# Kernel tuning notes

Measured on AMD Instinct MI355X. Metric: run time of the kernel, lower is better.

Reference implementation:

```python
import jax, jax.numpy as jnp
import numpy as np

N_WIRES = 4
DIM = 2 ** N_WIRES          # 16-dim state vector
N_OPS = 30                  # RandomLayer(n_ops=30)
GAMMA = 1.0
ALPHA = 0.5
C64 = jnp.complex64


def _rx_mat(t):
    h = t / 2
    c = jnp.cos(h).astype(C64)
    s = (-1j * jnp.sin(h)).astype(C64)
    return jnp.stack([jnp.stack([c, s]), jnp.stack([s, c])])


def _ry_mat(t):
    h = t / 2
    c = jnp.cos(h).astype(C64)
    s = jnp.sin(h).astype(C64)
    return jnp.stack([jnp.stack([c, -s]), jnp.stack([s, c])])


def _rz_mat(t):
    h = (t / 2).astype(C64)
    z = jnp.zeros((), C64)
    return jnp.stack([jnp.stack([jnp.exp(-1j * h), z]), jnp.stack([z, jnp.exp(1j * h)])])


def _embed(g, w):
    # kron(I_{2^w}, g, I_{2^{n-1-w}}); wire 0 = most significant qubit
    return jnp.kron(jnp.kron(jnp.eye(2 ** w, dtype=C64), g),
                    jnp.eye(2 ** (N_WIRES - 1 - w), dtype=C64))


def _cnot_full(c, t):
    m = np.zeros((DIM, DIM), np.complex64)
    for i in range(DIM):
        j = i ^ (1 << (N_WIRES - 1 - t)) if (i >> (N_WIRES - 1 - c)) & 1 else i
        m[j, i] = 1.0
    return jnp.asarray(m)


def fixed_unitary(rand_angles, rx_param, ry_param):
    """Compose the whole batch-independent gate sequence (random layer +
    per-wire trainable RX/RY) into one 16x16 unitary — the 'fused kernel'."""
    U = jnp.eye(DIM, dtype=C64)
    for i in range(N_OPS):
        t, w = i % 4, i % N_WIRES
        if t == 0:
            g = _embed(_rx_mat(rand_angles[i]), w)
        elif t == 1:
            g = _embed(_ry_mat(rand_angles[i]), w)
        elif t == 2:
            g = _embed(_rz_mat(rand_angles[i]), w)
        else:
            g = _cnot_full(w, (w + 1) % N_WIRES)
        U = g @ U
    for w in range(N_WIRES):
        U = _embed(_rx_mat(rx_param[0]), w) @ U
        U = _embed(_ry_mat(ry_param[0]), w) @ U
    return U


def encode_ry(state, angles):
    """GeneralEncoder '4xRy': apply RY(angles[:, w]) on wire w, batched."""
    B = state.shape[0]
    for w in range(N_WIRES):
        h = angles[:, w] / 2
        c = jnp.cos(h).astype(C64)[:, None, None]
        s = jnp.sin(h).astype(C64)[:, None, None]
        st = state.reshape(B, 2 ** w, 2, 2 ** (N_WIRES - 1 - w))
        s0, s1 = st[:, :, 0, :], st[:, :, 1, :]
        state = jnp.stack([c * s0 - s * s1, s * s0 + c * s1], axis=2).reshape(B, DIM)
    return state


def setup_inputs() -> dict:
    key = jax.random.key(0)
    k1, k2, k3, k4, k5 = jax.random.split(key, 5)
    B = 1048576
    return {
        "x": jax.random.normal(k1, (B, 4), dtype=jnp.float32),
        "y": jax.random.normal(k2, (B, 4), dtype=jnp.float32),
        "rand_angles": jax.random.uniform(k3, (30,), dtype=jnp.float32),
        "rx_param": jax.random.normal(k4, (1,), dtype=jnp.float32),
        "ry_param": jax.random.normal(k5, (1,), dtype=jnp.float32),
    }


def reference(x, y, rand_angles, rx_param, ry_param):
    B = x.shape[0]
    # classical RBF kernel, [B, 1]
    diff = x - y
    rbf = jnp.exp(-GAMMA * jnp.sum(diff * diff, axis=-1, keepdims=True))
    # quantum kernel: |0..0> -> encode(x) -> fixed unitary -> encode(-y)
    state = jnp.zeros((B, DIM), C64).at[:, 0].set(1.0)
    state = encode_ry(state, x)
    U = fixed_unitary(rand_angles, rx_param, ry_param)
    state = jnp.einsum('ij,bj->bi', U, state)
    state = encode_ry(state, -y)
    # torch: abs(states.view(-1)[0]) — first amplitude of first batch element
    qk = jnp.abs(state.reshape(-1)[0])
    return ALPHA * rbf + (1.0 - ALPHA) * qk
```

## Files before the change

### kernel.cpp

```cpp
#include <hip/hip_runtime.h>
#include <math.h>

#define DIM 16
#define N_OPS 30

__global__ __launch_bounds__(64) void build_qk_kernel(
    const float* __restrict__ x, const float* __restrict__ y,
    const float* __restrict__ rand_angles, const float* __restrict__ rx_param,
    const float* __restrict__ ry_param, float* __restrict__ qk_out) {
    const int lane = threadIdx.x;

    float h = 0.0f;
    if (lane < N_OPS)           h = 0.5f * rand_angles[lane];
    else if (lane == 30)        h = 0.5f * rx_param[0];
    else if (lane == 31)        h = 0.5f * ry_param[0];
    else if (lane >= 32 && lane < 36) h = 0.5f * x[lane - 32];
    else if (lane >= 36 && lane < 40) h = 0.5f * y[lane - 36];
    float sh_l, ch_l;
    __sincosf(h, &sh_l, &ch_l);

    float sr = 1.0f, si = 0.0f;
    #pragma unroll
    for (int w = 0; w < 4; ++w) {
        const int p = 3 - w;
        const float cw = __shfl(ch_l, 32 + w);
        const float sw = __shfl(sh_l, 32 + w);
        sr *= ((lane >> p) & 1) ? sw : cw;
    }

    #pragma unroll
    for (int i = 0; i < N_OPS; ++i) {
        const int t = i & 3;
        const float ch = __shfl(ch_l, i);
        const float sh = __shfl(sh_l, i);
        if (t == 0) {
            const float pr = __shfl_xor(sr, 8);
            const float pi = __shfl_xor(si, 8);
            const float nr = ch * sr + sh * pi;
            const float ni = ch * si - sh * pr;
            sr = nr; si = ni;
        } else if (t == 1) {
            const float pr = __shfl_xor(sr, 4);
            const float pi = __shfl_xor(si, 4);
            const float sg = ((lane >> 2) & 1) ? sh : -sh;
            const float nr = ch * sr + sg * pr;
            const float ni = ch * si + sg * pi;
            sr = nr; si = ni;
        } else if (t == 2) {
            const float sg = ((lane >> 1) & 1) ? sh : -sh;
            const float nr = ch * sr - sg * si;
            const float ni = ch * si + sg * sr;
            sr = nr; si = ni;
        } else {
            const float pr = __shfl_xor(sr, 8);
            const float pi = __shfl_xor(si, 8);
            if (lane & 1) { sr = pr; si = pi; }
        }
    }

    const float chx = __shfl(ch_l, 30), shx = __shfl(sh_l, 30);
    const float chy = __shfl(ch_l, 31), shy = __shfl(sh_l, 31);
    #pragma unroll
    for (int w = 0; w < 4; ++w) {
        const int p = 3 - w;
        {
            const float pr = __shfl_xor(sr, 1 << p);
            const float pi = __shfl_xor(si, 1 << p);
            const float nr = chx * sr + shx * pi;
            const float ni = chx * si - shx * pr;
            sr = nr; si = ni;
        }
        {
            const float pr = __shfl_xor(sr, 1 << p);
            const float pi = __shfl_xor(si, 1 << p);
            const float sg = ((lane >> p) & 1) ? shy : -shy;
            const float nr = chy * sr + sg * pr;
            const float ni = chy * si + sg * pi;
            sr = nr; si = ni;
        }
    }

    float wy = 1.0f;
    #pragma unroll
    for (int w = 0; w < 4; ++w) {
        const int p = 3 - w;
        const float cw = __shfl(ch_l, 36 + w);
        const float sw = __shfl(sh_l, 36 + w);
        wy *= ((lane >> p) & 1) ? sw : cw;
    }
    float ar = wy * sr;
    float ai = wy * si;
    #pragma unroll
    for (int m = 8; m >= 1; m >>= 1) {
        ar += __shfl_xor(ar, m);
        ai += __shfl_xor(ai, m);
    }
    if (lane == 0) qk_out[0] = sqrtf(ar * ar + ai * ai);
}

__global__ __launch_bounds__(256) void rbf_out_kernel(
    const float4* __restrict__ x, const float4* __restrict__ y,
    const float* __restrict__ qk_ptr, float* __restrict__ out, int B) {
    const int idx = blockIdx.x * blockDim.x + threadIdx.x;
    if (idx >= B) return;
    const float half_qk = 0.5f * qk_ptr[0];
    const float4 xv = x[idx];
    const float4 yv = y[idx];
    const float dx = xv.x - yv.x;
    const float dy = xv.y - yv.y;
    const float dz = xv.z - yv.z;
    const float dw = xv.w - yv.w;
    const float ss = dx * dx + dy * dy + dz * dz + dw * dw;
    out[idx] = 0.5f * expf(-ss) + half_qk;
}

extern "C" void kernel_launch(void* const* d_in, const int* in_sizes, int n_in,
                              void* d_out, int out_size, void* d_ws, size_t ws_size,
                              hipStream_t stream) {
    const float* x = (const float*)d_in[0];
    const float* y = (const float*)d_in[1];
    const float* rand_angles = (const float*)d_in[2];
    const float* rx_param = (const float*)d_in[3];
    const float* ry_param = (const float*)d_in[4];
    float* out = (float*)d_out;
    float* qk = (float*)d_ws;

    const int B = in_sizes[0] / 4;

    build_qk_kernel<<<1, 64, 0, stream>>>(x, y, rand_angles, rx_param, ry_param, qk);

    const int blocks = (B + 255) / 256;
    rbf_out_kernel<<<blocks, 256, 0, stream>>>(
        (const float4*)x, (const float4*)y, qk, out, B);
}
```

Baseline: 83.24 us.

## Fuse quantum-kernel scalar computation into RBF kernel, recomputed per block

Merges the single-wave quantum amplitude kernel and the elementwise RBF kernel into one launch. Every block's first wave recomputes the 16-amplitude state simulation redundantly and shares the result through shared memory, while the RBF values for two elements per thread are computed in parallel. This removes one kernel launch and the serial dependency between the two launches. The cost is redundant shuffle-heavy work and a block barrier in each of 2048 blocks. The change also switches expf to the fast __expf intrinsic, which lowers precision.

```diff
diff --git a/kernel.cpp b/kernel.cpp
--- a/kernel.cpp
+++ b/kernel.cpp
@@ -4,114 +4,127 @@
 #define DIM 16
 #define N_OPS 30
 
-__global__ __launch_bounds__(64) void build_qk_kernel(
+__global__ __launch_bounds__(256) void fused_hybrid_kernel(
+    const float4* __restrict__ x4, const float4* __restrict__ y4,
     const float* __restrict__ x, const float* __restrict__ y,
     const float* __restrict__ rand_angles, const float* __restrict__ rx_param,
-    const float* __restrict__ ry_param, float* __restrict__ qk_out) {
-    const int lane = threadIdx.x;
+    const float* __restrict__ ry_param, float* __restrict__ out, int B) {
+    __shared__ float s_qk;
 
-    float h = 0.0f;
-    if (lane < N_OPS)           h = 0.5f * rand_angles[lane];
-    else if (lane == 30)        h = 0.5f * rx_param[0];
-    else if (lane == 31)        h = 0.5f * ry_param[0];
-    else if (lane >= 32 && lane < 36) h = 0.5f * x[lane - 32];
-    else if (lane >= 36 && lane < 40) h = 0.5f * y[lane - 36];
-    float sh_l, ch_l;
-    __sincosf(h, &sh_l, &ch_l);
+    const int tid = threadIdx.x;
+    const int i0 = blockIdx.x * 512 + tid;
+    const int i1 = i0 + 256;
 
-    float sr = 1.0f, si = 0.0f;
-    #pragma unroll
-    for (int w = 0; w < 4; ++w) {
-        const int p = 3 - w;
-        const float cw = __shfl(ch_l, 32 + w);
-        const float sw = __shfl(sh_l, 32 + w);
-        sr *= ((lane >> p) & 1) ? sw : cw;
+    float r0 = 0.0f, r1 = 0.0f;
+    if (i0 < B) {
+        const float4 xv = x4[i0];
+        const float4 yv = y4[i0];
+        const float dx = xv.x - yv.x, dy = xv.y - yv.y;
+        const float dz = xv.z - yv.z, dw = xv.w - yv.w;
+        r0 = 0.5f * __expf(-(dx * dx + dy * dy + dz * dz + dw * dw));
+    }
+    if (i1 < B) {
+        const float4 xv = x4[i1];
+        const float4 yv = y4[i1];
+        const float dx = xv.x - yv.x, dy = xv.y - yv.y;
+        const float dz = xv.z - yv.z, dw = xv.w - yv.w;
+        r1 = 0.5f * __expf(-(dx * dx + dy * dy + dz * dz + dw * dw));
     }
 
-    #pragma unroll
-    for (int i = 0; i < N_OPS; ++i) {
-        const int t = i & 3;
-        const float ch = __shfl(ch_l, i);
-        const float sh = __shfl(sh_l, i);
-        if (t == 0) {
-            const float pr = __shfl_xor(sr, 8);
-            const float pi = __shfl_xor(si, 8);
-            const float nr = ch * sr + sh * pi;
-            const float ni = ch * si - sh * pr;
-            sr = nr; si = ni;
-        } else if (t == 1) {
-            const float pr = __shfl_xor(sr, 4);
-            const float pi = __shfl_xor(si, 4);
-            const float sg = ((lane >> 2) & 1) ? sh : -sh;
-            const float nr = ch * sr + sg * pr;
-            const float ni = ch * si + sg * pi;
-            sr = nr; si = ni;
-        } else if (t == 2) {
-            const float sg = ((lane >> 1) & 1) ? sh : -sh;
-            const float nr = ch * sr - sg * si;
-            const float ni = ch * si + sg * sr;
-            sr = nr; si = ni;
-        } else {
-            const float pr = __shfl_xor(sr, 8);
-            const float pi = __shfl_xor(si, 8);
-            if (lane & 1) { sr = pr; si = pi; }
+    if (tid < 64) {
+        const int lane = tid;
+        float h = 0.0f;
+        if (lane < N_OPS)                 h = 0.5f * rand_angles[lane];
+        else if (lane == 30)              h = 0.5f * rx_param[0];
+        else if (lane == 31)              h = 0.5f * ry_param[0];
+        else if (lane >= 32 && lane < 36) h = 0.5f * x[lane - 32];
+        else if (lane >= 36 && lane < 40) h = 0.5f * y[lane - 36];
+        float sh_l, ch_l;
+        __sincosf(h, &sh_l, &ch_l);
+
+        float sr = 1.0f, si = 0.0f;
+        #pragma unroll
+        for (int w = 0; w < 4; ++w) {
+            const int p = 3 - w;
+            const float cw = __shfl(ch_l, 32 + w);
+            const float sw = __shfl(sh_l, 32 + w);
+            sr *= ((lane >> p) & 1) ? sw : cw;
         }
+
+        #pragma unroll
+        for (int i = 0; i < N_OPS; ++i) {
+            const int t = i & 3;
+            const float ch = __shfl(ch_l, i);
+            const float sh = __shfl(sh_l, i);
+            if (t == 0) {
+                const float pr = __shfl_xor(sr, 8);
+                const float pi = __shfl_xor(si, 8);
+                const float nr = ch * sr + sh * pi;
+                const float ni = ch * si - sh * pr;
+                sr = nr; si = ni;
+            } else if (t == 1) {
+                const float pr = __shfl_xor(sr, 4);
+                const float pi = __shfl_xor(si, 4);
+                const float sg = ((lane >> 2) & 1) ? sh : -sh;
+                const float nr = ch * sr + sg * pr;
+                const float ni = ch * si + sg * pi;
+                sr = nr; si = ni;
+            } else if (t == 2) {
+                const float sg = ((lane >> 1) & 1) ? sh : -sh;
+                const float nr = ch * sr - sg * si;
+                const float ni = ch * si + sg * sr;
+                sr = nr; si = ni;
+            } else {
+                const float pr = __shfl_xor(sr, 8);
+                const float pi = __shfl_xor(si, 8);
+                if (lane & 1) { sr = pr; si = pi; }
+            }
+        }
+
+        const float chx = __shfl(ch_l, 30), shx = __shfl(sh_l, 30);
+        const float chy = __shfl(ch_l, 31), shy = __shfl(sh_l, 31);
+        #pragma unroll
+        for (int w = 0; w < 4; ++w) {
+            const int p = 3 - w;
+            {
+                const float pr = __shfl_xor(sr, 1 << p);
+                const float pi = __shfl_xor(si, 1 << p);
+                const float nr = chx * sr + shx * pi;
+                const float ni = chx * si - shx * pr;
+                sr = nr; si = ni;
+            }
+            {
+                const float pr = __shfl_xor(sr, 1 << p);
+                const float pi = __shfl_xor(si, 1 << p);
+                const float sg = ((lane >> p) & 1) ? shy : -shy;
+                const float nr = chy * sr + sg * pr;
+                const float ni = chy * si + sg * pi;
+                sr = nr; si = ni;
+            }
+        }
+
+        float wy = 1.0f;
+        #pragma unroll
+        for (int w = 0; w < 4; ++w) {
+            const int p = 3 - w;
+            const float cw = __shfl(ch_l, 36 + w);
+            const float sw = __shfl(sh_l, 36 + w);
+            wy *= ((lane >> p) & 1) ? sw : cw;
+        }
+        float ar = wy * sr;
+        float ai = wy * si;
+        #pragma unroll
+        for (int m = 8; m >= 1; m >>= 1) {
+            ar += __shfl_xor(ar, m);
+            ai += __shfl_xor(ai, m);
+        }
+        if (lane == 0) s_qk = 0.5f * sqrtf(ar * ar + ai * ai);
     }
+    __syncthreads();
 
-    const float chx = __shfl(ch_l, 30), shx = __shfl(sh_l, 30);
-    const float chy = __shfl(ch_l, 31), shy = __shfl(sh_l, 31);
-    #pragma unroll
-    for (int w = 0; w < 4; ++w) {
-        const int p = 3 - w;
-        {
-            const float pr = __shfl_xor(sr, 1 << p);
-            const float pi = __shfl_xor(si, 1 << p);
-            const float nr = chx * sr + shx * pi;
-            const float ni = chx * si - shx * pr;
-            sr = nr; si = ni;
-        }
-        {
-            const float pr = __shfl_xor(sr, 1 << p);
-            const float pi = __shfl_xor(si, 1 << p);
-            const float sg = ((lane >> p) & 1) ? shy : -shy;
-            const float nr = chy * sr + sg * pr;
-            const float ni = chy * si + sg * pi;
-            sr = nr; si = ni;
-        }
-    }
-
-    float wy = 1.0f;
-    #pragma unroll
-    for (int w = 0; w < 4; ++w) {
-        const int p = 3 - w;
-        const float cw = __shfl(ch_l, 36 + w);
-        const float sw = __shfl(sh_l, 36 + w);
-        wy *= ((lane >> p) & 1) ? sw : cw;
-    }
-    float ar = wy * sr;
-    float ai = wy * si;
-    #pragma unroll
-    for (int m = 8; m >= 1; m >>= 1) {
-        ar += __shfl_xor(ar, m);
-        ai += __shfl_xor(ai, m);
-    }
-    if (lane == 0) qk_out[0] = sqrtf(ar * ar + ai * ai);
-}
-
-__global__ __launch_bounds__(256) void rbf_out_kernel(
-    const float4* __restrict__ x, const float4* __restrict__ y,
-    const float* __restrict__ qk_ptr, float* __restrict__ out, int B) {
-    const int idx = blockIdx.x * blockDim.x + threadIdx.x;
-    if (idx >= B) return;
-    const float half_qk = 0.5f * qk_ptr[0];
-    const float4 xv = x[idx];
-    const float4 yv = y[idx];
-    const float dx = xv.x - yv.x;
-    const float dy = xv.y - yv.y;
-    const float dz = xv.z - yv.z;
-    const float dw = xv.w - yv.w;
-    const float ss = dx * dx + dy * dy + dz * dz + dw * dw;
-    out[idx] = 0.5f * expf(-ss) + half_qk;
+    const float hq = s_qk;
+    if (i0 < B) out[i0] = r0 + hq;
+    if (i1 < B) out[i1] = r1 + hq;
 }
 
 extern "C" void kernel_launch(void* const* d_in, const int* in_sizes, int n_in,
@@ -123,13 +136,11 @@
     const float* rx_param = (const float*)d_in[3];
     const float* ry_param = (const float*)d_in[4];
     float* out = (float*)d_out;
-    float* qk = (float*)d_ws;
 
     const int B = in_sizes[0] / 4;
+    const int blocks = (B + 511) / 512;
 
-    build_qk_kernel<<<1, 64, 0, stream>>>(x, y, rand_angles, rx_param, ry_param, qk);
-
-    const int blocks = (B + 255) / 256;
-    rbf_out_kernel<<<blocks, 256, 0, stream>>>(
-        (const float4*)x, (const float4*)y, qk, out, B);
+    fused_hybrid_kernel<<<blocks, 256, 0, stream>>>(
+        (const float4*)x, (const float4*)y, x, y,
+        rand_angles, rx_param, ry_param, out, B);
 }
```

Result: no change. 82.46 us (-0.9%).
